# Kernel tuning notes

Measured on AMD Instinct MI355X. Metric: run time of the kernel, lower is better.

The kernel has to match this reference:

```python
import jax, jax.numpy as jnp
import numpy as np

N_HEAD = 16


def setup_inputs() -> dict:
    key = jax.random.key(0)
    ks = jax.random.split(key, 9)
    b, s, d = 4, 2048, 1024
    scale = 1.0 / np.sqrt(d)
    return {
        "x": jax.random.normal(ks[0], (b, s, d), dtype=jnp.float32),
        "Wq": jax.random.normal(ks[1], (d, d), dtype=jnp.float32) * scale,
        "bq": jax.random.normal(ks[2], (d,), dtype=jnp.float32) * 0.01,
        "Wk": jax.random.normal(ks[3], (d, d), dtype=jnp.float32) * scale,
        "bk": jax.random.normal(ks[4], (d,), dtype=jnp.float32) * 0.01,
        "Wv": jax.random.normal(ks[5], (d, d), dtype=jnp.float32) * scale,
        "bv": jax.random.normal(ks[6], (d,), dtype=jnp.float32) * 0.01,
        "Wo": jax.random.normal(ks[7], (d, d), dtype=jnp.float32) * scale,
        "bo": jax.random.normal(ks[8], (d,), dtype=jnp.float32) * 0.01,
        "mask": 1,
    }


def reference(x, Wq, bq, Wk, bk, Wv, bv, Wo, bo, mask):
    b, s, d = x.shape
    h = N_HEAD
    dh = d // h
    # projections -> [b, h, s, dh]
    def proj(W, bias):
        return (x @ W + bias).reshape(b, s, h, dh).transpose(0, 2, 1, 3)

    Q = proj(Wq, bq)
    K = proj(Wk, bk)
    V = proj(Wv, bv)

    # full S x S scores (module materializes them explicitly)
    scores = jnp.einsum('bhqd,bhkd->bhqk', Q, K)
    if mask:
        causal = jnp.triu(jnp.ones((s, s), dtype=bool), k=1)
        scores = jnp.where(causal, -jnp.inf, scores)
    scores = scores / jnp.sqrt(jnp.asarray(dh, dtype=scores.dtype))
    attn = jax.nn.softmax(scores, axis=-1)
    out = jnp.einsum('bhqk,bhkd->bhqd', attn, V)  # [b, h, s, dh]
    out = out.transpose(0, 2, 1, 3).reshape(b, s, d)
    return out @ Wo + bo
```

## Files before the change

### kernel.cpp

```cpp
#include <hip/hip_runtime.h>

typedef unsigned short u16;
typedef unsigned int u32;
typedef __bf16 bf16x8 __attribute__((ext_vector_type(8)));
typedef float f32x4 __attribute__((ext_vector_type(4)));

#define BATCH 4
#define SLEN 2048
#define DMODEL 1024
#define NHEAD 16
#define DHEAD 64
#define MROWS (BATCH * SLEN)

__device__ __forceinline__ u16 f32_to_bf16(float f) {
  u32 u = __float_as_uint(f);
  u32 r = (u + 0x7FFFu + ((u >> 16) & 1u)) >> 16;
  return (u16)r;
}
__device__ __forceinline__ u32 pack_bf16x2(float a, float b) {
  return (u32)f32_to_bf16(a) | ((u32)f32_to_bf16(b) << 16);
}

__device__ __forceinline__ u32 pack_trunc(float lo, float hi) {
#if __has_builtin(__builtin_amdgcn_perm)
  return __builtin_amdgcn_perm(__float_as_uint(hi), __float_as_uint(lo), 0x07060302u);
#else
  return (__float_as_uint(hi) & 0xFFFF0000u) | (__float_as_uint(lo) >> 16);
#endif
}
__device__ __forceinline__ u32 pack_round(float lo, float hi) {
  u32 ul = __float_as_uint(lo) + 0x8000u;
  u32 uh = __float_as_uint(hi) + 0x8000u;
#if __has_builtin(__builtin_amdgcn_perm)
  return __builtin_amdgcn_perm(uh, ul, 0x07060302u);
#else
  return (uh & 0xFFFF0000u) | (ul >> 16);
#endif
}

#if __has_builtin(__builtin_amdgcn_exp2f)
#define EXP2(x) __builtin_amdgcn_exp2f(x)
#else
#define EXP2(x) exp2f(x)
#endif

typedef const __attribute__((address_space(1))) void* gas_cv;
typedef __attribute__((address_space(3))) void* las_v;
__device__ __forceinline__ void async16(const u16* g, u16* l) {
  __builtin_amdgcn_global_load_lds((gas_cv)g, (las_v)l, 16, 0, 0);
}


__global__ void convert_x_kernel(const float* __restrict__ x, u16* __restrict__ xb) {
  size_t i = ((size_t)blockIdx.x * 256 + threadIdx.x) * 8;
  float4 v0 = *(const float4*)(x + i);
  float4 v1 = *(const float4*)(x + i + 4);
  uint4 o;
  o.x = pack_bf16x2(v0.x, v0.y);
  o.y = pack_bf16x2(v0.z, v0.w);
  o.z = pack_bf16x2(v1.x, v1.y);
  o.w = pack_bf16x2(v1.z, v1.w);
  *(uint4*)(xb + i) = o;
}

__global__ void transpose_w_kernel(const float* __restrict__ Wq, const float* __restrict__ Wk,
                                   const float* __restrict__ Wv, const float* __restrict__ Wo,
                                   u16* __restrict__ wqkvt, u16* __restrict__ wot) {
  __shared__ float tile[32][33];
  int z = blockIdx.z;
  const float* src = (z == 0) ? Wq : (z == 1) ? Wk : (z == 2) ? Wv : Wo;
  u16* dst = (z < 3) ? (wqkvt + (size_t)z * DMODEL * DMODEL) : wot;
  int c0 = blockIdx.x * 32, r0 = blockIdx.y * 32;
  int tx = threadIdx.x & 31, ty = threadIdx.x >> 5;
#pragma unroll
  for (int i = 0; i < 4; ++i)
    tile[ty + 8 * i][tx] = src[(size_t)(r0 + ty + 8 * i) * DMODEL + c0 + tx];
  __syncthreads();
#pragma unroll
  for (int i = 0; i < 4; ++i)
    dst[(size_t)(c0 + ty + 8 * i) * DMODEL + r0 + tx] = f32_to_bf16(tile[tx][ty + 8 * i]);
}

__global__ void concat_bias_kernel(const float* __restrict__ bq, const float* __restrict__ bk,
                                   const float* __restrict__ bv, float* __restrict__ bqkv) {
  int i = blockIdx.x * 256 + threadIdx.x;
  float v = (i < 1024) ? bq[i] : (i < 2048) ? bk[i - 1024] : bv[i - 2048];
  bqkv[i] = v;
}

__global__ void transpose_v_kernel(const u16* __restrict__ qkv, u16* __restrict__ vt) {
  __shared__ u16 tile[32][33];
  const int bh = blockIdx.z;
  const int b = bh >> 4, h = bh & 15;
  const int s0 = blockIdx.x * 32, d0 = blockIdx.y * 32;
  const int tx = threadIdx.x & 31, ty = threadIdx.x >> 5;
#pragma unroll
  for (int i = 0; i < 4; ++i)
    tile[ty + 8 * i][tx] =
        qkv[(size_t)(b * SLEN + s0 + ty + 8 * i) * (3 * DMODEL) + 2 * DMODEL + h * DHEAD + d0 + tx];
  __syncthreads();
#pragma unroll
  for (int i = 0; i < 4; ++i)
    vt[(size_t)(bh * DHEAD + d0 + ty + 8 * i) * SLEN + s0 + tx] = tile[tx][ty + 8 * i];
}

template <int OUT_BF16>
__global__ __launch_bounds__(256) void gemm_bt_kernel(const u16* __restrict__ A,
                                                      const u16* __restrict__ Bt,
                                                      const float* __restrict__ bias,
                                                      void* __restrict__ Cout,
                                                      int M, int N, int K) {
  __shared__ u16 sA[128 * 32];
  __shared__ u16 sB[128 * 32];
  const int tid = threadIdx.x;
  const int wv = tid >> 6, lane = tid & 63;
  const int wr = wv >> 1, wc = wv & 1;
  const int col = lane & 15, quad = lane >> 4;
  const int m0 = blockIdx.x * 128;
  const int n0 = blockIdx.y * 128;

  f32x4 acc[4][4] = {};

  const int lr = tid >> 2;
  const int ls = tid & 3;
  const size_t a_base = (size_t)(m0 + lr) * K + ls * 8;
  const size_t b_base = (size_t)(n0 + lr) * K + ls * 8;
  u16* ldsA0 = sA + ((tid >> 6) << 9);
  u16* ldsA1 = ldsA0 + 2048;
  u16* ldsB0 = sB + ((tid >> 6) << 9);
  u16* ldsB1 = ldsB0 + 2048;

  for (int k0 = 0; k0 < K; k0 += 32) {
    async16(A + a_base + k0, ldsA0);
    async16(A + a_base + (size_t)64 * K + k0, ldsA1);
    async16(Bt + b_base + k0, ldsB0);
    async16(Bt + b_base + (size_t)64 * K + k0, ldsB1);
    __syncthreads();
    bf16x8 af[4], bfr[4];
#pragma unroll
    for (int i = 0; i < 4; ++i)
      af[i] = *(const bf16x8*)(sA + (wr * 64 + i * 16 + col) * 32 + quad * 8);
#pragma unroll
    for (int j = 0; j < 4; ++j)
      bfr[j] = *(const bf16x8*)(sB + (wc * 64 + j * 16 + col) * 32 + quad * 8);
#pragma unroll
    for (int i = 0; i < 4; ++i)
#pragma unroll
      for (int j = 0; j < 4; ++j)
        acc[i][j] = __builtin_amdgcn_mfma_f32_16x16x32_bf16(af[i], bfr[j], acc[i][j], 0, 0, 0);
    __syncthreads();
  }

#pragma unroll
  for (int i = 0; i < 4; ++i) {
#pragma unroll
    for (int j = 0; j < 4; ++j) {
      int n = n0 + wc * 64 + j * 16 + col;
      float bia = bias[n];
#pragma unroll
      for (int r = 0; r < 4; ++r) {
        int m = m0 + wr * 64 + i * 16 + quad * 4 + r;
        float v = acc[i][j][r] + bia;
        if (OUT_BF16)
          ((u16*)Cout)[(size_t)m * N + n] = f32_to_bf16(v);
        else
          ((float*)Cout)[(size_t)m * N + n] = v;
      }
    }
  }
}

__global__ __launch_bounds__(256, 4) void attn_kernel(const u16* __restrict__ qkv,
                                                      const u16* __restrict__ vt,
                                                      u16* __restrict__ out) {
  const int bh = blockIdx.y;
  const int b = bh >> 4, h = bh & 15;
  const int tid = threadIdx.x;
  const int wv = tid >> 6, lane = tid & 63;
  const int col = lane & 15, quad = lane >> 4;
  const int bx = blockIdx.x;
  const int sfirst = bx * 4 + wv;

  __shared__ u16 sK[2][64 * 64];
  __shared__ u16 sV[2][64 * 64];
  __shared__ u16 sP[4][16 * 64];
  u16* mysP = sP[wv];

  const u16* kbase = qkv + ((size_t)(b * SLEN)) * (3 * DMODEL) + DMODEL + h * DHEAD;
  const u16* vbase = vt + ((size_t)bh * DHEAD) * SLEN;
  const float scl2 = 0.125f * 1.44269504088896f;

  const int lrow = lane >> 3;
  const int sga = (lane & 7) ^ lrow;
  const int r0a = wv * 16, r0b = wv * 16 + 8;

  for (int half = 0; half < 2; ++half) {
    const int s2 = half ? (127 - sfirst) : sfirst;
    const int qbase = s2 * 16;
    const int nt = half ? (32 - bx) : (bx + 1);

    const u16* qrow = qkv + ((size_t)(b * SLEN + qbase + col)) * (3 * DMODEL) + h * DHEAD;
    bf16x8 aQ[2];
#pragma unroll
    for (int ks = 0; ks < 2; ++ks)
      aQ[ks] = *(const bf16x8*)(qrow + ks * 32 + quad * 8);

    f32x4 accO[4] = {};
    float m2 = -1e30f, l_i = 0.0f;

    async16(kbase + (size_t)(r0a + lrow) * (3 * DMODEL) + sga * 8, sK[0] + r0a * 64);
    async16(kbase + (size_t)(r0b + lrow) * (3 * DMODEL) + sga * 8, sK[0] + r0b * 64);
    async16(vbase + (size_t)(r0a + lrow) * SLEN + sga * 8, sV[0] + r0a * 64);
    async16(vbase + (size_t)(r0b + lrow) * SLEN + sga * 8, sV[0] + r0b * 64);

    for (int t = 0; t < nt; ++t) {
      const int kv0 = t * 64;
      const int cur = t & 1, nxt = cur ^ 1;

      if (t + 1 < nt) {
        const int kvn = kv0 + 64;
        async16(kbase + (size_t)(kvn + r0a + lrow) * (3 * DMODEL) + sga * 8, sK[nxt] + r0a * 64);
        async16(kbase + (size_t)(kvn + r0b + lrow) * (3 * DMODEL) + sga * 8, sK[nxt] + r0b * 64);
        async16(vbase + (size_t)(r0a + lrow) * SLEN + kvn + sga * 8, sV[nxt] + r0a * 64);
        async16(vbase + (size_t)(r0b + lrow) * SLEN + kvn + sga * 8, sV[nxt] + r0b * 64);
        asm volatile("s_waitcnt vmcnt(4)");
      } else {
        asm volatile("s_waitcnt vmcnt(0)");
      }
      __builtin_amdgcn_sched_barrier(0);
      __builtin_amdgcn_s_barrier();
      __builtin_amdgcn_sched_barrier(0);

      const u16* sKc = sK[cur];
      const u16* sVc = sV[cur];
      bf16x8 bK[2][4], bV[2][4];
#pragma unroll
      for (int ks = 0; ks < 2; ++ks) {
        const int sl = (((ks * 4 + quad) ^ (col & 7)) * 8);
#pragma unroll
        for (int cb = 0; cb < 4; ++cb)
          bK[ks][cb] = *(const bf16x8*)(sKc + (cb * 16 + col) * 64 + sl);
#pragma unroll
        for (int j = 0; j < 4; ++j)
          bV[ks][j] = *(const bf16x8*)(sVc + (j * 16 + col) * 64 + sl);
      }

      f32x4 accST[4] = {};
#pragma unroll
      for (int ks = 0; ks < 2; ++ks)
#pragma unroll
        for (int cb = 0; cb < 4; ++cb)
          accST[cb] = __builtin_amdgcn_mfma_f32_16x16x32_bf16(bK[ks][cb], aQ[ks],
                                                              accST[cb], 0, 0, 0);

      if (t == nt - 1) {
        int q = qbase + col;
#pragma unroll
        for (int cb = 0; cb < 4; ++cb) {
          int kvb = kv0 + cb * 16 + quad * 4;
#pragma unroll
          for (int r = 0; r < 4; ++r)
            if (kvb + r > q) accST[cb][r] = -1e30f;
        }
      }

      float ma = fmaxf(fmaxf(accST[0][0], accST[0][1]), fmaxf(accST[0][2], accST[0][3]));
      float mb = fmaxf(fmaxf(accST[1][0], accST[1][1]), fmaxf(accST[1][2], accST[1][3]));
      float mc = fmaxf(fmaxf(accST[2][0], accST[2][1]), fmaxf(accST[2][2], accST[2][3]));
      float md = fmaxf(fmaxf(accST[3][0], accST[3][1]), fmaxf(accST[3][2], accST[3][3]));
      float rmax = fmaxf(fmaxf(ma, mb), fmaxf(mc, md));
      rmax = fmaxf(rmax, __shfl_xor(rmax, 16));
      rmax = fmaxf(rmax, __shfl_xor(rmax, 32));
      float rmaxs = rmax * scl2;
      const bool noresc = __all(rmaxs <= m2);
      float mnew = noresc ? m2 : fmaxf(m2, rmaxs);
      float alpha = noresc ? 1.0f : EXP2(m2 - mnew);
      m2 = mnew;
      float sacc = 0.0f;
#pragma unroll
      for (int cb = 0; cb < 4; ++cb)
#pragma unroll
        for (int r = 0; r < 4; ++r) {
          float p = EXP2(__builtin_fmaf(accST[cb][r], scl2, -mnew));
          accST[cb][r] = p;
          sacc += p;
        }
      sacc += __shfl_xor(sacc, 16);
      sacc += __shfl_xor(sacc, 32);
      if (noresc) {
        l_i += sacc;
      } else {
        l_i = l_i * alpha + sacc;
#pragma unroll
        for (int j = 0; j < 4; ++j)
#pragma unroll
          for (int r = 0; r < 4; ++r) accO[j][r] *= alpha;
      }

#pragma unroll
      for (int cb = 0; cb < 4; ++cb) {
        uint2 pk;
        pk.x = pack_trunc(accST[cb][0], accST[cb][1]);
        pk.y = pack_trunc(accST[cb][2], accST[cb][3]);
        *(uint2*)(mysP + col * 64 + (((cb * 2 + (quad >> 1)) ^ (col & 7)) << 3) +
                  ((quad & 1) << 2)) = pk;
      }
      bf16x8 aP[2];
#pragma unroll
      for (int ks = 0; ks < 2; ++ks)
        aP[ks] = *(const bf16x8*)(mysP + col * 64 + (((ks * 4 + quad) ^ (col & 7)) << 3));

#pragma unroll
      for (int ks = 0; ks < 2; ++ks)
#pragma unroll
        for (int j = 0; j < 4; ++j)
          accO[j] = __builtin_amdgcn_mfma_f32_16x16x32_bf16(bV[ks][j], aP[ks],
                                                            accO[j], 0, 0, 0);

      __builtin_amdgcn_sched_barrier(0);
      __builtin_amdgcn_s_barrier();
      __builtin_amdgcn_sched_barrier(0);
    }

    {
      float rl = 1.0f / l_i;
      size_t rowoff = ((size_t)(b * SLEN + qbase + col)) * DMODEL + h * DHEAD;
#pragma unroll
      for (int j = 0; j < 4; ++j) {
        uint2 pk;
        pk.x = pack_round(accO[j][0] * rl, accO[j][1] * rl);
        pk.y = pack_round(accO[j][2] * rl, accO[j][3] * rl);
        *(uint2*)(out + rowoff + j * 16 + quad * 4) = pk;
      }
    }
  }
}


extern "C" void kernel_launch(void* const* d_in, const int* in_sizes, int n_in,
                              void* d_out, int out_size, void* d_ws, size_t ws_size,
                              hipStream_t stream) {
  const float* x = (const float*)d_in[0];
  const float* Wq = (const float*)d_in[1];
  const float* bq = (const float*)d_in[2];
  const float* Wk = (const float*)d_in[3];
  const float* bk = (const float*)d_in[4];
  const float* Wv = (const float*)d_in[5];
  const float* bv = (const float*)d_in[6];
  const float* Wo = (const float*)d_in[7];
  const float* bo = (const float*)d_in[8];

  char* ws = (char*)d_ws;
  u16* xb = (u16*)ws;
  u16* wqkvt = (u16*)(ws + ((size_t)16 << 20));
  u16* wot = (u16*)(ws + ((size_t)22 << 20));
  u16* qkv = (u16*)(ws + ((size_t)24 << 20));
  u16* attnO = (u16*)(ws + ((size_t)72 << 20));
  float* bqkv = (float*)(ws + ((size_t)88 << 20));
  u16* vtp = xb;

  convert_x_kernel<<<4096, 256, 0, stream>>>(x, xb);
  transpose_w_kernel<<<dim3(32, 32, 4), 256, 0, stream>>>(Wq, Wk, Wv, Wo, wqkvt, wot);
  concat_bias_kernel<<<12, 256, 0, stream>>>(bq, bk, bv, bqkv);
  gemm_bt_kernel<1><<<dim3(64, 24), 256, 0, stream>>>(xb, wqkvt, bqkv, (void*)qkv,
                                                      MROWS, 3 * DMODEL, DMODEL);
  transpose_v_kernel<<<dim3(64, 2, 64), 256, 0, stream>>>(qkv, vtp);
  attn_kernel<<<dim3(16, BATCH * NHEAD), 256, 0, stream>>>(qkv, vtp, attnO);
  gemm_bt_kernel<0><<<dim3(64, 8), 256, 0, stream>>>(attnO, wot, bo, d_out,
                                                     MROWS, DMODEL, DMODEL);
}
```

Before: 302.9 us.

## Switch attention to 32x32x16 MFMA tiles with 32-row query blocks per wave

Each wave in the attention kernel now handles 32 query rows using 32x32x16 bf16 MFMAs instead of 16 rows with 16x16x32. The P matrix is fed straight from accumulator registers into the PV MFMA, so the per-wave LDS round trip for P is gone. The grid is halved. Waves whose causal range ends early skip compute but still take part in the shared K/V loads and barriers. The cost is higher register pressure (launch bounds drop to 2) and idle waves in the tail tiles of each block.

Result: faster. 286.0 us (-5.6%).

```diff
diff --git a/kernel.cpp b/kernel.cpp
--- a/kernel.cpp
+++ b/kernel.cpp
@@ -2,8 +2,10 @@
 
 typedef unsigned short u16;
 typedef unsigned int u32;
+typedef __bf16 bf16x4 __attribute__((ext_vector_type(4)));
 typedef __bf16 bf16x8 __attribute__((ext_vector_type(8)));
 typedef float f32x4 __attribute__((ext_vector_type(4)));
+typedef float f32x16 __attribute__((ext_vector_type(16)));
 
 #define BATCH 4
 #define SLEN 2048
@@ -170,21 +172,19 @@
   }
 }
 
-__global__ __launch_bounds__(256, 4) void attn_kernel(const u16* __restrict__ qkv,
+__global__ __launch_bounds__(256, 2) void attn_kernel(const u16* __restrict__ qkv,
                                                       const u16* __restrict__ vt,
                                                       u16* __restrict__ out) {
   const int bh = blockIdx.y;
   const int b = bh >> 4, h = bh & 15;
   const int tid = threadIdx.x;
   const int wv = tid >> 6, lane = tid & 63;
-  const int col = lane & 15, quad = lane >> 4;
+  const int c = lane & 31, hi = lane >> 5;
   const int bx = blockIdx.x;
   const int sfirst = bx * 4 + wv;
 
   __shared__ u16 sK[2][64 * 64];
   __shared__ u16 sV[2][64 * 64];
-  __shared__ u16 sP[4][16 * 64];
-  u16* mysP = sP[wv];
 
   const u16* kbase = qkv + ((size_t)(b * SLEN)) * (3 * DMODEL) + DMODEL + h * DHEAD;
   const u16* vbase = vt + ((size_t)bh * DHEAD) * SLEN;
@@ -193,19 +193,21 @@
   const int lrow = lane >> 3;
   const int sga = (lane & 7) ^ lrow;
   const int r0a = wv * 16, r0b = wv * 16 + 8;
+  const int cs = c & 7;
 
   for (int half = 0; half < 2; ++half) {
-    const int s2 = half ? (127 - sfirst) : sfirst;
-    const int qbase = s2 * 16;
-    const int nt = half ? (32 - bx) : (bx + 1);
-
-    const u16* qrow = qkv + ((size_t)(b * SLEN + qbase + col)) * (3 * DMODEL) + h * DHEAD;
-    bf16x8 aQ[2];
-#pragma unroll
-    for (int ks = 0; ks < 2; ++ks)
-      aQ[ks] = *(const bf16x8*)(qrow + ks * 32 + quad * 8);
-
-    f32x4 accO[4] = {};
+    const int s2 = half ? (63 - sfirst) : sfirst;
+    const int qbase = s2 * 32;
+    const int nt_own = s2 / 2 + 1;
+    const int nt = half ? (32 - 2 * bx) : (2 * bx + 2);
+
+    const u16* qrow =
+        qkv + ((size_t)(b * SLEN + qbase + c)) * (3 * DMODEL) + h * DHEAD + hi * 8;
+    bf16x8 aQ[4];
+#pragma unroll
+    for (int ks = 0; ks < 4; ++ks) aQ[ks] = *(const bf16x8*)(qrow + ks * 16);
+
+    f32x16 accO[2] = {};
     float m2 = -1e30f, l_i = 0.0f;
 
     async16(kbase + (size_t)(r0a + lrow) * (3 * DMODEL) + sga * 8, sK[0] + r0a * 64);
@@ -231,91 +233,113 @@
       __builtin_amdgcn_s_barrier();
       __builtin_amdgcn_sched_barrier(0);
 
-      const u16* sKc = sK[cur];
-      const u16* sVc = sV[cur];
-      bf16x8 bK[2][4], bV[2][4];
-#pragma unroll
-      for (int ks = 0; ks < 2; ++ks) {
-        const int sl = (((ks * 4 + quad) ^ (col & 7)) * 8);
-#pragma unroll
-        for (int cb = 0; cb < 4; ++cb)
-          bK[ks][cb] = *(const bf16x8*)(sKc + (cb * 16 + col) * 64 + sl);
-#pragma unroll
-        for (int j = 0; j < 4; ++j)
-          bV[ks][j] = *(const bf16x8*)(sVc + (j * 16 + col) * 64 + sl);
+      if (t < nt_own) {
+        const u16* sKc = sK[cur];
+        const u16* sVc = sV[cur];
+        bf16x8 bK[2][4], bV[2][4];
+#pragma unroll
+        for (int m = 0; m < 2; ++m) {
+          const int rb = (m * 32 + c) * 64;
+#pragma unroll
+          for (int ks = 0; ks < 4; ++ks) {
+            bK[m][ks] = *(const bf16x8*)(sKc + rb + (((ks * 2 + hi) ^ cs) << 3));
+            bf16x4 vlo = *(const bf16x4*)(sVc + rb + (((ks * 2) ^ cs) << 3) + 4 * hi);
+            bf16x4 vhi = *(const bf16x4*)(sVc + rb + (((ks * 2 + 1) ^ cs) << 3) + 4 * hi);
+            bV[m][ks] = __builtin_shufflevector(vlo, vhi, 0, 1, 2, 3, 4, 5, 6, 7);
+          }
+        }
+
+        f32x16 accST[2] = {};
+#pragma unroll
+        for (int ks = 0; ks < 4; ++ks)
+#pragma unroll
+          for (int m = 0; m < 2; ++m)
+            accST[m] = __builtin_amdgcn_mfma_f32_32x32x16_bf16(bK[m][ks], aQ[ks],
+                                                               accST[m], 0, 0, 0);
+
+        if (t == nt_own - 1) {
+          const int q = qbase + c;
+          const int kvh = kv0 + 4 * hi;
+#pragma unroll
+          for (int m = 0; m < 2; ++m)
+#pragma unroll
+            for (int r = 0; r < 16; ++r) {
+              int kv = kvh + m * 32 + ((r & 3) + 8 * (r >> 2));
+              if (kv > q) accST[m][r] = -1e30f;
+            }
+        }
+
+        float h0 = fmaxf(fmaxf(accST[0][0], accST[0][1]), fmaxf(accST[0][2], accST[0][3]));
+        float h1 = fmaxf(fmaxf(accST[0][4], accST[0][5]), fmaxf(accST[0][6], accST[0][7]));
+        float h2 = fmaxf(fmaxf(accST[0][8], accST[0][9]), fmaxf(accST[0][10], accST[0][11]));
+        float h3 = fmaxf(fmaxf(accST[0][12], accST[0][13]), fmaxf(accST[0][14], accST[0][15]));
+        float h4 = fmaxf(fmaxf(accST[1][0], accST[1][1]), fmaxf(accST[1][2], accST[1][3]));
+        float h5 = fmaxf(fmaxf(accST[1][4], accST[1][5]), fmaxf(accST[1][6], accST[1][7]));
+        float h6 = fmaxf(fmaxf(accST[1][8], accST[1][9]), fmaxf(accST[1][10], accST[1][11]));
+        float h7 = fmaxf(fmaxf(accST[1][12], accST[1][13]), fmaxf(accST[1][14], accST[1][15]));
+        float rmax = fmaxf(fmaxf(fmaxf(h0, h1), fmaxf(h2, h3)),
+                           fmaxf(fmaxf(h4, h5), fmaxf(h6, h7)));
+        rmax = fmaxf(rmax, __shfl_xor(rmax, 32));
+        float rmaxs = rmax * scl2;
+        const bool noresc = __all(rmaxs <= m2);
+        float mnew = noresc ? m2 : fmaxf(m2, rmaxs);
+        float alpha = noresc ? 1.0f : EXP2(m2 - mnew);
+        m2 = mnew;
+
+        float s0 = 0.f, s1 = 0.f, s2s = 0.f, s3 = 0.f;
+#pragma unroll
+        for (int m = 0; m < 2; ++m) {
+#pragma unroll
+          for (int r = 0; r < 16; r += 4) {
+            float p0 = EXP2(__builtin_fmaf(accST[m][r + 0], scl2, -mnew));
+            float p1 = EXP2(__builtin_fmaf(accST[m][r + 1], scl2, -mnew));
+            float p2 = EXP2(__builtin_fmaf(accST[m][r + 2], scl2, -mnew));
+            float p3 = EXP2(__builtin_fmaf(accST[m][r + 3], scl2, -mnew));
+            accST[m][r + 0] = p0;
+            accST[m][r + 1] = p1;
+            accST[m][r + 2] = p2;
+            accST[m][r + 3] = p3;
+            s0 += p0;
+            s1 += p1;
+            s2s += p2;
+            s3 += p3;
+          }
+        }
+        float sacc = (s0 + s1) + (s2s + s3);
+        sacc += __shfl_xor(sacc, 32);
+        if (noresc) {
+          l_i += sacc;
+        } else {
+          l_i = l_i * alpha + sacc;
+#pragma unroll
+          for (int m = 0; m < 2; ++m)
+#pragma unroll
+            for (int r = 0; r < 16; ++r) accO[m][r] *= alpha;
+        }
+
+        bf16x8 aP[4];
+#pragma unroll
+        for (int m = 0; m < 2; ++m)
+#pragma unroll
+          for (int s = 0; s < 2; ++s) {
+            union {
+              uint4 u;
+              bf16x8 v;
+            } cvt;
+            cvt.u.x = pack_trunc(accST[m][8 * s + 0], accST[m][8 * s + 1]);
+            cvt.u.y = pack_trunc(accST[m][8 * s + 2], accST[m][8 * s + 3]);
+            cvt.u.z = pack_trunc(accST[m][8 * s + 4], accST[m][8 * s + 5]);
+            cvt.u.w = pack_trunc(accST[m][8 * s + 6], accST[m][8 * s + 7]);
+            aP[m * 2 + s] = cvt.v;
+          }
+
+#pragma unroll
+        for (int ks = 0; ks < 4; ++ks)
+#pragma unroll
+          for (int m = 0; m < 2; ++m)
+            accO[m] = __builtin_amdgcn_mfma_f32_32x32x16_bf16(bV[m][ks], aP[ks],
+                                                              accO[m], 0, 0, 0);
       }
-
-      f32x4 accST[4] = {};
-#pragma unroll
-      for (int ks = 0; ks < 2; ++ks)
-#pragma unroll
-        for (int cb = 0; cb < 4; ++cb)
-          accST[cb] = __builtin_amdgcn_mfma_f32_16x16x32_bf16(bK[ks][cb], aQ[ks],
-                                                              accST[cb], 0, 0, 0);
-
-      if (t == nt - 1) {
-        int q = qbase + col;
-#pragma unroll
-        for (int cb = 0; cb < 4; ++cb) {
-          int kvb = kv0 + cb * 16 + quad * 4;
-#pragma unroll
-          for (int r = 0; r < 4; ++r)
-            if (kvb + r > q) accST[cb][r] = -1e30f;
-        }
-      }
-
-      float ma = fmaxf(fmaxf(accST[0][0], accST[0][1]), fmaxf(accST[0][2], accST[0][3]));
-      float mb = fmaxf(fmaxf(accST[1][0], accST[1][1]), fmaxf(accST[1][2], accST[1][3]));
-      float mc = fmaxf(fmaxf(accST[2][0], accST[2][1]), fmaxf(accST[2][2], accST[2][3]));
-      float md = fmaxf(fmaxf(accST[3][0], accST[3][1]), fmaxf(accST[3][2], accST[3][3]));
-      float rmax = fmaxf(fmaxf(ma, mb), fmaxf(mc, md));
-      rmax = fmaxf(rmax, __shfl_xor(rmax, 16));
-      rmax = fmaxf(rmax, __shfl_xor(rmax, 32));
-      float rmaxs = rmax * scl2;
-      const bool noresc = __all(rmaxs <= m2);
-      float mnew = noresc ? m2 : fmaxf(m2, rmaxs);
-      float alpha = noresc ? 1.0f : EXP2(m2 - mnew);
-      m2 = mnew;
-      float sacc = 0.0f;
-#pragma unroll
-      for (int cb = 0; cb < 4; ++cb)
-#pragma unroll
-        for (int r = 0; r < 4; ++r) {
-          float p = EXP2(__builtin_fmaf(accST[cb][r], scl2, -mnew));
-          accST[cb][r] = p;
-          sacc += p;
-        }
-      sacc += __shfl_xor(sacc, 16);
-      sacc += __shfl_xor(sacc, 32);
-      if (noresc) {
-        l_i += sacc;
-      } else {
-        l_i = l_i * alpha + sacc;
-#pragma unroll
-        for (int j = 0; j < 4; ++j)
-#pragma unroll
-          for (int r = 0; r < 4; ++r) accO[j][r] *= alpha;
-      }
-
-#pragma unroll
-      for (int cb = 0; cb < 4; ++cb) {
-        uint2 pk;
-        pk.x = pack_trunc(accST[cb][0], accST[cb][1]);
-        pk.y = pack_trunc(accST[cb][2], accST[cb][3]);
-        *(uint2*)(mysP + col * 64 + (((cb * 2 + (quad >> 1)) ^ (col & 7)) << 3) +
-                  ((quad & 1) << 2)) = pk;
-      }
-      bf16x8 aP[2];
-#pragma unroll
-      for (int ks = 0; ks < 2; ++ks)
-        aP[ks] = *(const bf16x8*)(mysP + col * 64 + (((ks * 4 + quad) ^ (col & 7)) << 3));
-
-#pragma unroll
-      for (int ks = 0; ks < 2; ++ks)
-#pragma unroll
-        for (int j = 0; j < 4; ++j)
-          accO[j] = __builtin_amdgcn_mfma_f32_16x16x32_bf16(bV[ks][j], aP[ks],
-                                                            accO[j], 0, 0, 0);
 
       __builtin_amdgcn_sched_barrier(0);
       __builtin_amdgcn_s_barrier();
@@ -324,14 +348,17 @@
 
     {
       float rl = 1.0f / l_i;
-      size_t rowoff = ((size_t)(b * SLEN + qbase + col)) * DMODEL + h * DHEAD;
-#pragma unroll
-      for (int j = 0; j < 4; ++j) {
-        uint2 pk;
-        pk.x = pack_round(accO[j][0] * rl, accO[j][1] * rl);
-        pk.y = pack_round(accO[j][2] * rl, accO[j][3] * rl);
-        *(uint2*)(out + rowoff + j * 16 + quad * 4) = pk;
-      }
+      size_t rowoff =
+          ((size_t)(b * SLEN + qbase + c)) * DMODEL + h * DHEAD + 4 * hi;
+#pragma unroll
+      for (int m = 0; m < 2; ++m)
+#pragma unroll
+        for (int j = 0; j < 4; ++j) {
+          uint2 pk;
+          pk.x = pack_round(accO[m][4 * j + 0] * rl, accO[m][4 * j + 1] * rl);
+          pk.y = pack_round(accO[m][4 * j + 2] * rl, accO[m][4 * j + 3] * rl);
+          *(uint2*)(out + rowoff + m * 32 + 8 * j) = pk;
+        }
     }
   }
 }
@@ -365,7 +392,7 @@
   gemm_bt_kernel<1><<<dim3(64, 24), 256, 0, stream>>>(xb, wqkvt, bqkv, (void*)qkv,
                                                       MROWS, 3 * DMODEL, DMODEL);
   transpose_v_kernel<<<dim3(64, 2, 64), 256, 0, stream>>>(qkv, vtp);
-  attn_kernel<<<dim3(16, BATCH * NHEAD), 256, 0, stream>>>(qkv, vtp, attnO);
+  attn_kernel<<<dim3(8, BATCH * NHEAD), 256, 0, stream>>>(qkv, vtp, attnO);
   gemm_bt_kernel<0><<<dim3(64, 8), 256, 0, stream>>>(attnO, wot, bo, d_out,
                                                      MROWS, DMODEL, DMODEL);
 }
```
